# Performance work log

Hardware: AMD Instinct MI355X
Metric: run time of the kernel (lower is better)

Reference implementation:

```python
import jax, jax.numpy as jnp
import numpy as np
from jax import lax

WIN = 9  # window size per spatial dim


def setup_inputs() -> dict:
    key = jax.random.key(0)
    k1, k2 = jax.random.split(key)
    shape = (2, 1, 160, 192, 160)  # [B, C=1, D, H, W]
    y_true = jax.random.uniform(k1, shape, dtype=jnp.float32)
    y_pred = jax.random.uniform(k2, shape, dtype=jnp.float32)
    return {"y_true": y_true, "y_pred": y_pred}


def reference(y_true, y_pred):
    Ii, Ji = y_true, y_pred
    ndims = Ii.ndim - 2  # 3 for volumes
    pad = WIN // 2
    # all five maps in the channel dim: [B, 5, D, H, W]
    all_five = jnp.concatenate([Ii, Ji, Ii * Ii, Ji * Ji, Ii * Ji], axis=1)
    # grouped box-filter conv: ones kernel [O=5, I/g=1, 9,9,9]
    kernel = jnp.ones((5, 1) + (WIN,) * ndims, dtype=Ii.dtype)
    conv = lax.conv_general_dilated(
        all_five, kernel,
        window_strides=(1,) * ndims,
        padding=[(pad, pad)] * ndims,
        feature_group_count=5,
        dimension_numbers=("NCDHW", "OIDHW", "NCDHW"),
    )
    I_sum, J_sum, I2_sum, J2_sum, IJ_sum = jnp.split(conv, 5, axis=1)
    win_size = jnp.asarray(float(WIN), dtype=Ii.dtype)
    cross = IJ_sum - J_sum / win_size * I_sum
    I_var = I2_sum - I_sum / win_size * I_sum
    J_var = J2_sum - J_sum / win_size * J_sum
    cc = cross * cross / (I_var * J_var + 1e-5)
    return -jnp.mean(cc)
```

## Files before the change

kernel.cpp:

```cpp
#include <hip/hip_runtime.h>

#define B_ 2
#define D_ 160
#define H_ 192
#define W_ 160
#define HW_ (H_ * W_)
#define DHW_ (D_ * HW_)
#define NV_ ((long long)B_ * D_ * H_ * W_)

#define YH1 48
#define NYH (H_ / YH1)
#define SROWS (YH1 + 8)
#define SSTRH (W_ + 4)
#define YCH1 6

#define ROWS2 8
#define ZCH2 10
#define NZC2 (D_ / ZCH2)
#define LROW 168

#define RW_ 168
#define A_Y ((size_t)5 * RW_)
#define A_Z ((size_t)H_ * A_Y)

typedef _Float16 half4 __attribute__((ext_vector_type(4)));

__global__ void k_zero(double* acc) { *acc = 0.0; }

__device__ __forceinline__ void add4h(float4& d, const half4 v) {
    d.x += (float)v.x; d.y += (float)v.y; d.z += (float)v.z; d.w += (float)v.w;
}
__device__ __forceinline__ void sub4h(float4& d, const half4 v) {
    d.x -= (float)v.x; d.y -= (float)v.y; d.z -= (float)v.z; d.w -= (float)v.w;
}

template<int SGN>
__device__ __forceinline__ void accPr(float4 s[5], const half4 ha, const half4 hb) {
    const float4 a = make_float4((float)ha.x, (float)ha.y, (float)ha.z, (float)ha.w);
    const float4 b = make_float4((float)hb.x, (float)hb.y, (float)hb.z, (float)hb.w);
    if (SGN > 0) {
        s[0].x += a.x;     s[0].y += a.y;     s[0].z += a.z;     s[0].w += a.w;
        s[1].x += b.x;     s[1].y += b.y;     s[1].z += b.z;     s[1].w += b.w;
        s[2].x += a.x*a.x; s[2].y += a.y*a.y; s[2].z += a.z*a.z; s[2].w += a.w*a.w;
        s[3].x += b.x*b.x; s[3].y += b.y*b.y; s[3].z += b.z*b.z; s[3].w += b.w*b.w;
        s[4].x += a.x*b.x; s[4].y += a.y*b.y; s[4].z += a.z*b.z; s[4].w += a.w*b.w;
    } else {
        s[0].x -= a.x;     s[0].y -= a.y;     s[0].z -= a.z;     s[0].w -= a.w;
        s[1].x -= b.x;     s[1].y -= b.y;     s[1].z -= b.z;     s[1].w -= b.w;
        s[2].x -= a.x*a.x; s[2].y -= a.y*a.y; s[2].z -= a.z*a.z; s[2].w -= a.w*a.w;
        s[3].x -= b.x*b.x; s[3].y -= b.y*b.y; s[3].z -= b.z*b.z; s[3].w -= b.w*b.w;
        s[4].x -= a.x*b.x; s[4].y -= a.y*b.y; s[4].z -= a.z*b.z; s[4].w -= a.w*b.w;
    }
}

__global__ __launch_bounds__(320) void k1_ysum(const float* __restrict__ I,
                                               const float* __restrict__ J,
                                               _Float16* __restrict__ A) {
    __shared__ _Float16 sI[SROWS][SSTRH];
    __shared__ _Float16 sJ[SROWS][SSTRH];
    const int tid = threadIdx.x;
    const int yh  = blockIdx.x % NYH;
    const int bz  = blockIdx.x / NYH;
    const int ylo = yh * YH1 - 4;

    const float* Ib = I + (size_t)bz * HW_;
    const float* Jb = J + (size_t)bz * HW_;

#pragma unroll
    for (int i = 0; i < 7; ++i) {
        const int idx = i * 320 + tid;
        const int lr  = idx / 40;
        const int g   = idx - lr * 40;
        const int gy  = ylo + lr;
        half4 hi, hj;
        hi.x = hi.y = hi.z = hi.w = (_Float16)0.f;
        hj.x = hj.y = hj.z = hj.w = (_Float16)0.f;
        if (gy >= 0 && gy < H_) {
            const float4 vi = *(const float4*)(Ib + (size_t)gy * W_ + g * 4);
            const float4 vj = *(const float4*)(Jb + (size_t)gy * W_ + g * 4);
            hi.x = (_Float16)vi.x; hi.y = (_Float16)vi.y; hi.z = (_Float16)vi.z; hi.w = (_Float16)vi.w;
            hj.x = (_Float16)vj.x; hj.y = (_Float16)vj.y; hj.z = (_Float16)vj.z; hj.w = (_Float16)vj.w;
        }
        *(half4*)&sI[lr][g * 4] = hi;
        *(half4*)&sJ[lr][g * 4] = hj;
    }
    __syncthreads();

    const int xg = tid % 40;
    const int yc = tid / 40;
    const int x4 = xg * 4;
    const int y0 = yh * YH1 + yc * YCH1;
    const int l0 = yc * YCH1 + 4;

    _Float16* Ap = A + (size_t)bz * A_Z;

    float4 s[5];
#pragma unroll
    for (int c = 0; c < 5; ++c) s[c] = make_float4(0.f, 0.f, 0.f, 0.f);

#pragma unroll
    for (int j = 0; j < 8; ++j)
        accPr<+1>(s, *(const half4*)&sI[l0 - 4 + j][x4], *(const half4*)&sJ[l0 - 4 + j][x4]);

    half4 zer;
    zer.x = zer.y = zer.z = zer.w = (_Float16)0.f;

#pragma unroll
    for (int k = 0; k < YCH1; ++k) {
        const int ll = l0 + k + 4;
        accPr<+1>(s, *(const half4*)&sI[ll][x4], *(const half4*)&sJ[ll][x4]);
        if (k >= 1) {
            const int lt = l0 + k - 5;
            accPr<-1>(s, *(const half4*)&sI[lt][x4], *(const half4*)&sJ[lt][x4]);
        }
        _Float16* Ay = Ap + (size_t)(y0 + k) * A_Y;
#pragma unroll
        for (int c = 0; c < 5; ++c) {
            half4 h;
            h.x = (_Float16)s[c].x; h.y = (_Float16)s[c].y;
            h.z = (_Float16)s[c].z; h.w = (_Float16)s[c].w;
            *(half4*)(Ay + c * RW_ + 4 + x4) = h;
            if (xg == 0)  *(half4*)(Ay + c * RW_)       = zer;
            if (xg == 39) *(half4*)(Ay + c * RW_ + 164) = zer;
        }
    }
}

__device__ __forceinline__ float cc4(const float4 S0, const float4 S1, const float4 S2,
                                     const float4 S3, const float4 S4) {
    const float inv9 = 1.0f / 9.0f;
    float a = 0.f;
    { const float cr = S4.x - S1.x * S0.x * inv9;
      const float iv = S2.x - S0.x * S0.x * inv9;
      const float jv = S3.x - S1.x * S1.x * inv9;
      a += cr * cr / (iv * jv + 1e-5f); }
    { const float cr = S4.y - S1.y * S0.y * inv9;
      const float iv = S2.y - S0.y * S0.y * inv9;
      const float jv = S3.y - S1.y * S1.y * inv9;
      a += cr * cr / (iv * jv + 1e-5f); }
    { const float cr = S4.z - S1.z * S0.z * inv9;
      const float iv = S2.z - S0.z * S0.z * inv9;
      const float jv = S3.z - S1.z * S1.z * inv9;
      a += cr * cr / (iv * jv + 1e-5f); }
    { const float cr = S4.w - S1.w * S0.w * inv9;
      const float iv = S2.w - S0.w * S0.w * inv9;
      const float jv = S3.w - S1.w * S1.w * inv9;
      a += cr * cr / (iv * jv + 1e-5f); }
    return a;
}

__global__ __launch_bounds__(320) void k2_zxcc(const _Float16* __restrict__ A,
                                               double* __restrict__ acc) {
    __shared__ float sbuf[ROWS2][5][LROW];
    __shared__ float red[512];
    const int tid = threadIdx.x;
    const int r   = tid / 40;
    const int xg  = tid - r * 40;
    const int x4  = xg * 4;
    const int blk = blockIdx.x;
    const int zc  = blk % NZC2;
    const int rp  = blk / NZC2;
    const int gy  = rp * ROWS2 + r;
    const int b   = gy / H_;
    const int yy  = gy - b * H_;
    const int z0  = zc * ZCH2;

    {
        float* p = &sbuf[0][0][0];
        for (int i = tid; i < ROWS2 * 5 * LROW; i += 320) p[i] = 0.f;
    }

    const _Float16* Abase = A + (size_t)(b * D_) * A_Z + (size_t)yy * A_Y + 4 + x4;

    float4 s[5];
#pragma unroll
    for (int c = 0; c < 5; ++c) s[c] = make_float4(0.f, 0.f, 0.f, 0.f);
#pragma unroll
    for (int j = 0; j < 9; ++j) {
        const int zi = z0 - 5 + j;
        if (zi >= 0) {
            const _Float16* Az = Abase + (size_t)zi * A_Z;
            add4h(s[0], *(const half4*)(Az + 0 * RW_));
            add4h(s[1], *(const half4*)(Az + 1 * RW_));
            add4h(s[2], *(const half4*)(Az + 2 * RW_));
            add4h(s[3], *(const half4*)(Az + 3 * RW_));
            add4h(s[4], *(const half4*)(Az + 4 * RW_));
        }
    }
    __syncthreads();

    float local = 0.f;
    for (int k = 0; k < ZCH2; ++k) {
        const int zi = z0 + k + 4;
        if (zi < D_) {
            const _Float16* Az = Abase + (size_t)zi * A_Z;
            add4h(s[0], *(const half4*)(Az + 0 * RW_));
            add4h(s[1], *(const half4*)(Az + 1 * RW_));
            add4h(s[2], *(const half4*)(Az + 2 * RW_));
            add4h(s[3], *(const half4*)(Az + 3 * RW_));
            add4h(s[4], *(const half4*)(Az + 4 * RW_));
        }
        const int zo = z0 + k - 5;
        if (zo >= 0) {
            const _Float16* Az = Abase + (size_t)zo * A_Z;
            sub4h(s[0], *(const half4*)(Az + 0 * RW_));
            sub4h(s[1], *(const half4*)(Az + 1 * RW_));
            sub4h(s[2], *(const half4*)(Az + 2 * RW_));
            sub4h(s[3], *(const half4*)(Az + 3 * RW_));
            sub4h(s[4], *(const half4*)(Az + 4 * RW_));
        }
        *(float4*)&sbuf[r][0][4 + x4] = s[0];
        *(float4*)&sbuf[r][1][4 + x4] = s[1];
        *(float4*)&sbuf[r][2][4 + x4] = s[2];
        *(float4*)&sbuf[r][3][4 + x4] = s[3];
        *(float4*)&sbuf[r][4][4 + x4] = s[4];
        __syncthreads();

        float4 S5[5];
#pragma unroll
        for (int c = 0; c < 5; ++c) {
            const float4 a0 = *(const float4*)&sbuf[r][c][x4];
            const float4 a1 = *(const float4*)&sbuf[r][c][x4 + 4];
            const float4 a2 = *(const float4*)&sbuf[r][c][x4 + 8];
            const float o0 = a0.x + a0.y + a0.z + a0.w + a1.x + a1.y + a1.z + a1.w + a2.x;
            const float o1 = o0 - a0.x + a2.y;
            const float o2 = o1 - a0.y + a2.z;
            const float o3 = o2 - a0.z + a2.w;
            S5[c] = make_float4(o0, o1, o2, o3);
        }
        local += cc4(S5[0], S5[1], S5[2], S5[3], S5[4]);
        __syncthreads();
    }

    red[tid] = local;
    if (tid < 192) red[320 + tid] = 0.f;
    __syncthreads();
    for (int off = 256; off > 0; off >>= 1) {
        if (tid < off) red[tid] += red[tid + off];
        __syncthreads();
    }
    if (tid == 0) atomicAdd(acc, (double)red[0]);
}

__global__ void p_direct(const float* __restrict__ I, const float* __restrict__ J,
                         double* __restrict__ acc) {
    const long long idx = (long long)blockIdx.x * blockDim.x + threadIdx.x;
    float local = 0.f;
    if (idx < NV_) {
        const int x = (int)(idx % W_);
        long long t = idx / W_;
        const int y = (int)(t % H_);
        t /= H_;
        const int z = (int)(t % D_);
        const int b = (int)(t / D_);
        const int z0 = max(z - 4, 0), z1 = min(z + 4, D_ - 1);
        const int y0 = max(y - 4, 0), y1 = min(y + 4, H_ - 1);
        const int x0 = max(x - 4, 0), x1 = min(x + 4, W_ - 1);
        float sI = 0.f, sJ = 0.f, sI2 = 0.f, sJ2 = 0.f, sIJ = 0.f;
        for (int zz = z0; zz <= z1; ++zz)
            for (int yy = y0; yy <= y1; ++yy) {
                const size_t row = ((size_t)(b * D_ + zz) * H_ + yy) * W_;
                for (int xx = x0; xx <= x1; ++xx) {
                    const float a = I[row + xx];
                    const float bb = J[row + xx];
                    sI += a; sJ += bb; sI2 += a * a; sJ2 += bb * bb; sIJ += a * bb;
                }
            }
        const float inv9 = 1.0f / 9.0f;
        const float cross = sIJ - sJ * sI * inv9;
        const float iv    = sI2 - sI * sI * inv9;
        const float jv    = sJ2 - sJ * sJ * inv9;
        local = cross * cross / (iv * jv + 1e-5f);
    }
    __shared__ float red[256];
    red[threadIdx.x] = local;
    __syncthreads();
    for (int off = 128; off > 0; off >>= 1) {
        if (threadIdx.x < off) red[threadIdx.x] += red[threadIdx.x + off];
        __syncthreads();
    }
    if (threadIdx.x == 0) atomicAdd(acc, (double)red[0]);
}

__global__ void k_final(const double* __restrict__ acc, float* __restrict__ out) {
    out[0] = (float)(-(*acc) / (double)NV_);
}

extern "C" void kernel_launch(void* const* d_in, const int* in_sizes, int n_in,
                              void* d_out, int out_size, void* d_ws, size_t ws_size,
                              hipStream_t stream) {
    const float* I = (const float*)d_in[0];
    const float* J = (const float*)d_in[1];
    float* out = (float*)d_out;

    const size_t needA = (size_t)B_ * D_ * A_Z * sizeof(_Float16);
    if (ws_size >= 1024 + needA) {
        double* acc = (double*)d_ws;
        _Float16* A = (_Float16*)((char*)d_ws + 1024);
        k_zero<<<1, 1, 0, stream>>>(acc);
        k1_ysum<<<B_ * D_ * NYH, 320, 0, stream>>>(I, J, A);
        k2_zxcc<<<NZC2 * (B_ * H_ / ROWS2), 320, 0, stream>>>(A, acc);
        k_final<<<1, 1, 0, stream>>>(acc, out);
    } else if (ws_size >= sizeof(double)) {
        double* acc = (double*)d_ws;
        k_zero<<<1, 1, 0, stream>>>(acc);
        p_direct<<<(int)((NV_ + 255) / 256), 256, 0, stream>>>(I, J, acc);
        k_final<<<1, 1, 0, stream>>>(acc, out);
    }
}
```

Baseline: 92.57 us.

## Double-buffer fp16 shared rows in zx pass and drop second barrier

The zx pass now stores its per-row partial sums in shared memory as fp16 and ping-pongs between two buffers. This lets it drop the trailing __syncthreads in each z iteration and halves shared-memory traffic for the x-window. The y-pass tile height shrinks from 48 to 32 rows, which gives more blocks and less shared memory per block but more halo overhead. The fp16 rounding of z-summed values (up to 81 products) adds precision loss to the correlation terms.

Measured after the change: 95.61 us. +3.3%, slower.

```diff
diff --git a/kernel.cpp b/kernel.cpp
--- a/kernel.cpp
+++ b/kernel.cpp
@@ -8,16 +8,15 @@
 #define DHW_ (D_ * HW_)
 #define NV_ ((long long)B_ * D_ * H_ * W_)
 
-#define YH1 48
+#define YH1 32
 #define NYH (H_ / YH1)
 #define SROWS (YH1 + 8)
 #define SSTRH (W_ + 4)
-#define YCH1 6
+#define YCH1 4
 
 #define ROWS2 8
 #define ZCH2 10
 #define NZC2 (D_ / ZCH2)
-#define LROW 168
 
 #define RW_ 168
 #define A_Y ((size_t)5 * RW_)
@@ -27,6 +26,9 @@
 
 __global__ void k_zero(double* acc) { *acc = 0.0; }
 
+__device__ __forceinline__ float4 h2f(const half4 h) {
+    return make_float4((float)h.x, (float)h.y, (float)h.z, (float)h.w);
+}
 __device__ __forceinline__ void add4h(float4& d, const half4 v) {
     d.x += (float)v.x; d.y += (float)v.y; d.z += (float)v.z; d.w += (float)v.w;
 }
@@ -36,8 +38,8 @@
 
 template<int SGN>
 __device__ __forceinline__ void accPr(float4 s[5], const half4 ha, const half4 hb) {
-    const float4 a = make_float4((float)ha.x, (float)ha.y, (float)ha.z, (float)ha.w);
-    const float4 b = make_float4((float)hb.x, (float)hb.y, (float)hb.z, (float)hb.w);
+    const float4 a = h2f(ha);
+    const float4 b = h2f(hb);
     if (SGN > 0) {
         s[0].x += a.x;     s[0].y += a.y;     s[0].z += a.z;     s[0].w += a.w;
         s[1].x += b.x;     s[1].y += b.y;     s[1].z += b.z;     s[1].w += b.w;
@@ -67,7 +69,7 @@
     const float* Jb = J + (size_t)bz * HW_;
 
 #pragma unroll
-    for (int i = 0; i < 7; ++i) {
+    for (int i = 0; i < 5; ++i) {
         const int idx = i * 320 + tid;
         const int lr  = idx / 40;
         const int g   = idx - lr * 40;
@@ -151,7 +153,7 @@
 
 __global__ __launch_bounds__(320) void k2_zxcc(const _Float16* __restrict__ A,
                                                double* __restrict__ acc) {
-    __shared__ float sbuf[ROWS2][5][LROW];
+    __shared__ _Float16 sbuf[2][ROWS2][5][RW_];
     __shared__ float red[512];
     const int tid = threadIdx.x;
     const int r   = tid / 40;
@@ -166,8 +168,8 @@
     const int z0  = zc * ZCH2;
 
     {
-        float* p = &sbuf[0][0][0];
-        for (int i = tid; i < ROWS2 * 5 * LROW; i += 320) p[i] = 0.f;
+        _Float16* p = &sbuf[0][0][0][0];
+        for (int i = tid; i < 2 * ROWS2 * 5 * RW_; i += 320) p[i] = (_Float16)0.f;
     }
 
     const _Float16* Abase = A + (size_t)(b * D_) * A_Z + (size_t)yy * A_Y + 4 + x4;
@@ -209,19 +211,22 @@
             sub4h(s[3], *(const half4*)(Az + 3 * RW_));
             sub4h(s[4], *(const half4*)(Az + 4 * RW_));
         }
-        *(float4*)&sbuf[r][0][4 + x4] = s[0];
-        *(float4*)&sbuf[r][1][4 + x4] = s[1];
-        *(float4*)&sbuf[r][2][4 + x4] = s[2];
-        *(float4*)&sbuf[r][3][4 + x4] = s[3];
-        *(float4*)&sbuf[r][4][4 + x4] = s[4];
+        const int p = k & 1;
+#pragma unroll
+        for (int c = 0; c < 5; ++c) {
+            half4 h;
+            h.x = (_Float16)s[c].x; h.y = (_Float16)s[c].y;
+            h.z = (_Float16)s[c].z; h.w = (_Float16)s[c].w;
+            *(half4*)&sbuf[p][r][c][4 + x4] = h;
+        }
         __syncthreads();
 
         float4 S5[5];
 #pragma unroll
         for (int c = 0; c < 5; ++c) {
-            const float4 a0 = *(const float4*)&sbuf[r][c][x4];
-            const float4 a1 = *(const float4*)&sbuf[r][c][x4 + 4];
-            const float4 a2 = *(const float4*)&sbuf[r][c][x4 + 8];
+            const float4 a0 = h2f(*(const half4*)&sbuf[p][r][c][x4]);
+            const float4 a1 = h2f(*(const half4*)&sbuf[p][r][c][x4 + 4]);
+            const float4 a2 = h2f(*(const half4*)&sbuf[p][r][c][x4 + 8]);
             const float o0 = a0.x + a0.y + a0.z + a0.w + a1.x + a1.y + a1.z + a1.w + a2.x;
             const float o1 = o0 - a0.x + a2.y;
             const float o2 = o1 - a0.y + a2.z;
@@ -229,7 +234,6 @@
             S5[c] = make_float4(o0, o1, o2, o3);
         }
         local += cc4(S5[0], S5[1], S5[2], S5[3], S5[4]);
-        __syncthreads();
     }
 
     red[tid] = local;
```
